# Kernel tuning notes

Measured on AMD Instinct MI355X. Metric: run time of the kernel, lower is better.

## Reference

```python
import jax, jax.numpy as jnp
import numpy as np

N_NODES = 50000
N_EDGES = 800000
IN_DIM = 128
OUT_DIM = 64
NEG_SLOPE = 0.2  # PyG GATConv default negative_slope


def setup_inputs() -> dict:
    key = jax.random.key(0)
    k1, k2, k3, k4, k5, k6 = jax.random.split(key, 6)
    x = jax.random.normal(k1, (N_NODES, IN_DIM), dtype=jnp.float32)
    edge_index = jax.random.randint(k2, (2, N_EDGES), 0, N_NODES, dtype=jnp.int32)
    # GATConv params (heads=1): linear weight, attention vectors, bias
    s = 1.0 / np.sqrt(IN_DIM)
    W = jax.random.uniform(k3, (IN_DIM, OUT_DIM), jnp.float32, -s, s)
    att_src = jax.random.normal(k4, (OUT_DIM,), jnp.float32) * 0.1
    att_dst = jax.random.normal(k5, (OUT_DIM,), jnp.float32) * 0.1
    bias = jnp.zeros((OUT_DIM,), jnp.float32)
    return {"x": x, "edge_index": edge_index, "W": W,
            "att_src": att_src, "att_dst": att_dst, "bias": bias}


def reference(x, edge_index, W, att_src, att_dst, bias):
    N = x.shape[0]
    h = x @ W  # [N, F_out]
    # add self loops (PyG GATConv default)
    loop = jnp.arange(N, dtype=edge_index.dtype)
    src = jnp.concatenate([edge_index[0], loop])  # message sources j
    dst = jnp.concatenate([edge_index[1], loop])  # aggregation targets i
    # per-node attention logits, gathered per edge
    a_src = h @ att_src  # [N]
    a_dst = h @ att_dst  # [N]
    e = jax.nn.leaky_relu(a_src[src] + a_dst[dst], NEG_SLOPE)  # [E+N]
    # scatter-softmax over incoming edges of each dst node
    m = jax.ops.segment_max(e, dst, num_segments=N)  # [N]
    ex = jnp.exp(e - m[dst])
    denom = jax.ops.segment_sum(ex, dst, num_segments=N)  # [N], >0 due to self loops
    alpha = ex / denom[dst]  # [E+N]
    # gather-weight-scatter aggregate
    out = jax.ops.segment_sum(h[src] * alpha[:, None], dst, num_segments=N)
    return out + bias
```

## Files before the change

### kernel.cpp

```cpp
#include <hip/hip_runtime.h>
#include <hip/hip_fp16.h>

#define NN 50000
#define NE 800000
#define IN_DIM 128
#define OUT_DIM 64
#define NEG 0.2f

#define BSHIFT 7
#define BNODES 128
#define NBUCK 391
#define HALFCAP 2560
#define CHUNK 4096
#define BIN_BLOCKS 196
#define GEMM_BLOCKS 391

#define XS_STRIDE 136

typedef short short8 __attribute__((ext_vector_type(8)));
typedef float f32x4 __attribute__((ext_vector_type(4)));

__device__ __forceinline__ unsigned short f2bf(float f) {
    unsigned u = __float_as_uint(f);
    u += 0x7FFFu + ((u >> 16) & 1u);
    return (unsigned short)(u >> 16);
}

__global__ __launch_bounds__(512) void gat_zero(int* __restrict__ bucket_cur) {
    if (threadIdx.x < NBUCK) bucket_cur[threadIdx.x] = 0;
}

__global__ __launch_bounds__(512) void gat_gemm_bin(
    const float* __restrict__ x, const float* __restrict__ W,
    const float* __restrict__ att_src, const float* __restrict__ att_dst,
    const int* __restrict__ src, const int* __restrict__ dst,
    unsigned short* __restrict__ h2, float* __restrict__ a_src,
    float* __restrict__ a_dst,
    int* __restrict__ gbucket, int* __restrict__ bucket_cur)
{
    __shared__ __align__(16) unsigned short xs[128 * XS_STRIDE];
    __shared__ __align__(16) unsigned short wt[64 * XS_STRIDE];
    const int tid = threadIdx.x;
    const int lane = tid & 63, wid = tid >> 6;

    if (blockIdx.x < BIN_BLOCKS) {
        int* recs_in  = (int*)xs;
        int* bcnt     = recs_in + CHUNK;
        int* cur      = bcnt + 512;
        int* lbase    = cur + 512;
        int* comb     = lbase + 512;
        int* wsum     = comb + 512;
        int* recs_out = (int*)wt;
        const int e0 = blockIdx.x * CHUNK;
        const int total = (e0 + CHUNK < NE ? CHUNK : NE - e0);

        bcnt[tid] = 0;
        __syncthreads();
#pragma unroll
        for (int k = 0; k < CHUNK / 512; ++k) {
            const int e = e0 + k * 512 + tid;
            if (e < NE) {
                const int d = dst[e];
                const int bkt = d >> BSHIFT;
                recs_in[k * 512 + tid] =
                    (bkt << 23) | (src[e] << BSHIFT) | (d & (BNODES - 1));
                atomicAdd(&bcnt[bkt], 1);
            }
        }
        __syncthreads();
        const int v = bcnt[tid];
        int incl = v;
#pragma unroll
        for (int off = 1; off < 64; off <<= 1) {
            const int n = __shfl_up(incl, off, 64);
            if (lane >= off) incl += n;
        }
        if (lane == 63) wsum[wid] = incl;
        __syncthreads();
        int wpre = 0;
#pragma unroll
        for (int w = 0; w < 8; ++w)
            if (w < wid) wpre += wsum[w];
        const int excl = wpre + incl - v;
        lbase[tid] = excl; cur[tid] = excl;
        int gb = 0;
        if (tid < NBUCK && v) gb = atomicAdd(&bucket_cur[tid], v);
        comb[tid] = gb - excl;
        __syncthreads();
#pragma unroll
        for (int k = 0; k < CHUNK / 512; ++k) {
            const int idx = k * 512 + tid;
            if (idx < total) {
                const int r = recs_in[idx];
                const unsigned bkt = (unsigned)r >> 23;
                const int pos = atomicAdd(&cur[bkt], 1);
                recs_out[pos] = r;
            }
        }
        __syncthreads();
        for (int j = tid; j < total; j += 512) {
            const int r = recs_out[j];
            const unsigned bkt = (unsigned)r >> 23;
            const int rel = comb[bkt] + j;
            if (rel < HALFCAP)
                gbucket[bkt * HALFCAP + rel] = r & 0x7FFFFF;
        }
        return;
    }

    const int block_row = (blockIdx.x - BIN_BLOCKS) * 128;

    for (int t = tid; t < 128 * 32; t += 512) {
        const int r = t >> 5, k = (t & 31) << 2;
        const int row = block_row + r;
        float4 v = make_float4(0.f, 0.f, 0.f, 0.f);
        if (row < NN) v = *(const float4*)(x + (size_t)row * IN_DIM + k);
        ushort4 p;
        p.x = f2bf(v.x); p.y = f2bf(v.y); p.z = f2bf(v.z); p.w = f2bf(v.w);
        *(ushort4*)&xs[r * XS_STRIDE + k] = p;
    }
    for (int t = tid; t < 128 * 16; t += 512) {
        const int k = t >> 4, n4 = (t & 15) << 2;
        const float4 v = *(const float4*)(W + k * 64 + n4);
        wt[(n4 + 0) * XS_STRIDE + k] = f2bf(v.x);
        wt[(n4 + 1) * XS_STRIDE + k] = f2bf(v.y);
        wt[(n4 + 2) * XS_STRIDE + k] = f2bf(v.z);
        wt[(n4 + 3) * XS_STRIDE + k] = f2bf(v.w);
    }
    __syncthreads();

    const int m = lane & 15, quad = lane >> 4;

    f32x4 acc[4];
#pragma unroll
    for (int ct = 0; ct < 4; ++ct) acc[ct] = (f32x4){0.f, 0.f, 0.f, 0.f};

    const unsigned short* xrow = &xs[(wid * 16 + m) * XS_STRIDE + quad * 8];
#pragma unroll
    for (int kt = 0; kt < 4; ++kt) {
        short8 af = *(const short8*)(xrow + kt * 32);
#pragma unroll
        for (int ct = 0; ct < 4; ++ct) {
            short8 bf = *(const short8*)(&wt[(ct * 16 + m) * XS_STRIDE + kt * 32 + quad * 8]);
            acc[ct] = __builtin_amdgcn_mfma_f32_16x16x32_bf16(af, bf, acc[ct], 0, 0, 0);
        }
    }

    float as_c[4], ad_c[4];
#pragma unroll
    for (int ct = 0; ct < 4; ++ct) {
        as_c[ct] = att_src[ct * 16 + m];
        ad_c[ct] = att_dst[ct * 16 + m];
    }
    float ps[4], pd[4];
#pragma unroll
    for (int reg = 0; reg < 4; ++reg) {
        float s = 0.f, d = 0.f;
#pragma unroll
        for (int ct = 0; ct < 4; ++ct) {
            s += acc[ct][reg] * as_c[ct];
            d += acc[ct][reg] * ad_c[ct];
        }
        ps[reg] = s; pd[reg] = d;
    }
#pragma unroll
    for (int off = 1; off < 16; off <<= 1) {
#pragma unroll
        for (int reg = 0; reg < 4; ++reg) {
            ps[reg] += __shfl_xor(ps[reg], off, 64);
            pd[reg] += __shfl_xor(pd[reg], off, 64);
        }
    }
    if (m == 0) {
#pragma unroll
        for (int reg = 0; reg < 4; ++reg) {
            const int row = block_row + wid * 16 + quad * 4 + reg;
            if (row < NN) { a_src[row] = ps[reg]; a_dst[row] = pd[reg]; }
        }
    }

    __syncthreads();
    unsigned short* hs = xs;
#pragma unroll
    for (int ct = 0; ct < 4; ++ct)
#pragma unroll
        for (int reg = 0; reg < 4; ++reg)
            hs[(wid * 16 + quad * 4 + reg) * 72 + ct * 16 + m] =
                __half_as_ushort(__float2half(acc[ct][reg]));
    __syncthreads();
    {
        const int r = tid >> 2, c = (tid & 3) * 16;
        const int row = block_row + r;
        if (row < NN) {
            uint4 v0 = *(const uint4*)&hs[r * 72 + c];
            uint4 v1 = *(const uint4*)&hs[r * 72 + c + 8];
            *(uint4*)(h2 + (size_t)row * 64 + c) = v0;
            *(uint4*)(h2 + (size_t)row * 64 + c + 8) = v1;
        }
    }
}

__global__ __launch_bounds__(1024) void gat_sortagg(
    const int* __restrict__ gbucket, const int* __restrict__ bucket_cur,
    const __half* __restrict__ h2, const float* __restrict__ a_src,
    const float* __restrict__ a_dst, const float* __restrict__ bias,
    float* __restrict__ out)
{
    __shared__ int raw[HALFCAP];
    __shared__ unsigned srtex[HALFCAP];
    __shared__ int hist[BNODES];
    __shared__ int scanb[BNODES];
    __shared__ int cur[BNODES];
    __shared__ float ads[BNODES];
    __shared__ float ass[BNODES];
    __shared__ int wsum[2];
    const int b = blockIdx.x;
    const int tid = threadIdx.x;
    const int node0 = b << BSHIFT;

    int cnt_b = bucket_cur[b];
    if (cnt_b > HALFCAP) cnt_b = HALFCAP;
    const int* win = gbucket + (size_t)b * HALFCAP;

    if (tid < BNODES) {
        hist[tid] = 0;
        const int n = node0 + tid;
        ads[tid] = (n < NN) ? a_dst[n] : 0.f;
        ass[tid] = (n < NN) ? a_src[n] : 0.f;
    }
    __syncthreads();
    for (int i = tid; i < cnt_b; i += 1024) {
        const int r = win[i];
        raw[i] = r;
        atomicAdd(&hist[r & (BNODES - 1)], 1);
    }
    __syncthreads();
    const int lane = tid & 63;
    int v = 0, incl = 0;
    if (tid < BNODES) {
        v = hist[tid];
        incl = v;
#pragma unroll
        for (int off = 1; off < 64; off <<= 1) {
            const int n = __shfl_up(incl, off, 64);
            if (lane >= off) incl += n;
        }
        if (lane == 63) wsum[tid >> 6] = incl;
    }
    __syncthreads();
    if (tid < BNODES) {
        const int inclT = incl + ((tid >= 64) ? wsum[0] : 0);
        scanb[tid] = inclT;
        cur[tid] = inclT - v;
    }
    __syncthreads();
    for (int i = tid; i < cnt_b; i += 1024) {
        const int r = raw[i];
        const int dl = r & (BNODES - 1);
        const int s = (r >> BSHIFT) & 0xFFFF;
        float ev = a_src[s] + ads[dl];
        ev = ev > 0.f ? ev : NEG * ev;
        const float ex = __expf(ev);
        const int pos = atomicAdd(&cur[dl], 1);
        srtex[pos] = (unsigned)s |
                     ((unsigned)__half_as_ushort(__float2half(ex)) << 16);
    }
    __syncthreads();

    const int wid = tid >> 6;
    const int grp = lane >> 3;
    const int cq = lane & 7;

    for (int k = 0; k < 8; ++k) {
        const int ln = k * 16 + wid;
        const int node = node0 + ln;
        if (node >= NN) break;
        const int deg = hist[ln];
        const int rbase = scanb[ln] - deg;

        float v2 = ass[ln] + ads[ln];
        v2 = v2 > 0.f ? v2 : NEG * v2;
        const float exs = __expf(v2);
        const float w0 = (grp == 0) ? exs : 0.f;

        uint4 hp = *(const uint4*)(h2 + ((size_t)node << 6) + (cq << 3));

        int   sA = -1; float eA = 0.f; uint4 gA = make_uint4(0, 0, 0, 0);
        int   sB = -1; float eB = 0.f; uint4 gB = make_uint4(0, 0, 0, 0);
        if (grp < deg) {
            const unsigned p = srtex[rbase + grp];
            sA = (int)(p & 0xffffu);
            eA = __half2float(__ushort_as_half((unsigned short)(p >> 16)));
            gA = *(const uint4*)(h2 + ((size_t)sA << 6) + (cq << 3));
        }
        if (8 + grp < deg) {
            const unsigned p = srtex[rbase + 8 + grp];
            sB = (int)(p & 0xffffu);
            eB = __half2float(__ushort_as_half((unsigned short)(p >> 16)));
            gB = *(const uint4*)(h2 + ((size_t)sB << 6) + (cq << 3));
        }

        float acc[8];
        {
            const __half2* hh = (const __half2*)&hp;
#pragma unroll
            for (int j = 0; j < 4; ++j) {
                float2 f = __half22float2(hh[j]);
                acc[2 * j] = w0 * f.x;
                acc[2 * j + 1] = w0 * f.y;
            }
        }
        float den = w0;

        for (int base = 0; base < deg; base += 8) {
            int sC = -1; float eC = 0.f; uint4 gC = make_uint4(0, 0, 0, 0);
            const int en = base + 16 + grp;
            if (en < deg) {
                const unsigned p = srtex[rbase + en];
                sC = (int)(p & 0xffffu);
                eC = __half2float(__ushort_as_half((unsigned short)(p >> 16)));
                gC = *(const uint4*)(h2 + ((size_t)sC << 6) + (cq << 3));
            }
            if (sA >= 0) {
                const __half2* gh = (const __half2*)&gA;
#pragma unroll
                for (int j = 0; j < 4; ++j) {
                    float2 f = __half22float2(gh[j]);
                    acc[2 * j] += eA * f.x;
                    acc[2 * j + 1] += eA * f.y;
                }
                den += eA;
            }
            sA = sB; eA = eB; gA = gB;
            sB = sC; eB = eC; gB = gC;
        }

#pragma unroll
        for (int off = 8; off < 64; off <<= 1) {
#pragma unroll
            for (int j = 0; j < 8; ++j) acc[j] += __shfl_xor(acc[j], off, 64);
            den += __shfl_xor(den, off, 64);
        }

        if (grp == 0) {
            const float inv = 1.f / den;
            const float4 b0 = *(const float4*)(bias + (cq << 3));
            const float4 b1 = *(const float4*)(bias + (cq << 3) + 4);
            float4 o0, o1;
            o0.x = acc[0] * inv + b0.x; o0.y = acc[1] * inv + b0.y;
            o0.z = acc[2] * inv + b0.z; o0.w = acc[3] * inv + b0.w;
            o1.x = acc[4] * inv + b1.x; o1.y = acc[5] * inv + b1.y;
            o1.z = acc[6] * inv + b1.z; o1.w = acc[7] * inv + b1.w;
            float* op = out + ((size_t)node << 6) + (cq << 3);
            *(float4*)op = o0;
            *(float4*)(op + 4) = o1;
        }
    }
}

extern "C" void kernel_launch(void* const* d_in, const int* in_sizes, int n_in,
                              void* d_out, int out_size, void* d_ws, size_t ws_size,
                              hipStream_t stream) {
    const float* x       = (const float*)d_in[0];
    const int*   eidx    = (const int*)d_in[1];
    const float* W       = (const float*)d_in[2];
    const float* att_src = (const float*)d_in[3];
    const float* att_dst = (const float*)d_in[4];
    const float* bias    = (const float*)d_in[5];
    float* out = (float*)d_out;

    unsigned short* h2 = (unsigned short*)d_ws;
    int*   gbucket = (int*)((char*)d_ws + (size_t)NN * OUT_DIM * 2);
    float* a_src   = (float*)(gbucket + (size_t)NBUCK * HALFCAP);
    float* a_dst   = a_src + NN;
    int*   bucket_cur = (int*)(a_dst + NN);

    const int* src = eidx;
    const int* dst = eidx + NE;

    gat_zero<<<1, 512, 0, stream>>>(bucket_cur);
    gat_gemm_bin<<<GEMM_BLOCKS + BIN_BLOCKS, 512, 0, stream>>>(
        x, W, att_src, att_dst, src, dst, h2, a_src, a_dst, gbucket, bucket_cur);
    gat_sortagg<<<NBUCK, 1024, 0, stream>>>(
        gbucket, bucket_cur, (const __half*)h2, a_src, a_dst, bias, out);
}
```

Measured before the change: 125.7 us.

## Assign one 8-lane group per node instead of one wave per node in aggregation

The aggregation phase previously used one 64-lane wave per destination node, with eight 8-lane groups splitting the node's edges and a cross-group shuffle reduction at the end. Now each 8-lane group owns one node (128 nodes across the 1024-thread block) and walks all of that node's edges serially, prefetching two edges ahead. This removes the shuffle reduction and the idle lanes on low-degree nodes (average degree is about 16). In exchange, each lane runs a longer serial loop, and work becomes imbalanced across lanes within a wave when node degrees differ.

Measured after the change: 113.1 us. -10.0%, faster.

```diff
diff --git a/kernel.cpp b/kernel.cpp
--- a/kernel.cpp
+++ b/kernel.cpp
@@ -267,82 +267,69 @@
     }
     __syncthreads();
 
-    const int wid = tid >> 6;
-    const int grp = lane >> 3;
-    const int cq = lane & 7;
-
-    for (int k = 0; k < 8; ++k) {
-        const int ln = k * 16 + wid;
-        const int node = node0 + ln;
-        if (node >= NN) break;
-        const int deg = hist[ln];
-        const int rbase = scanb[ln] - deg;
-
-        float v2 = ass[ln] + ads[ln];
-        v2 = v2 > 0.f ? v2 : NEG * v2;
-        const float exs = __expf(v2);
-        const float w0 = (grp == 0) ? exs : 0.f;
-
-        uint4 hp = *(const uint4*)(h2 + ((size_t)node << 6) + (cq << 3));
-
-        int   sA = -1; float eA = 0.f; uint4 gA = make_uint4(0, 0, 0, 0);
-        int   sB = -1; float eB = 0.f; uint4 gB = make_uint4(0, 0, 0, 0);
-        if (grp < deg) {
-            const unsigned p = srtex[rbase + grp];
-            sA = (int)(p & 0xffffu);
-            eA = __half2float(__ushort_as_half((unsigned short)(p >> 16)));
-            gA = *(const uint4*)(h2 + ((size_t)sA << 6) + (cq << 3));
-        }
-        if (8 + grp < deg) {
-            const unsigned p = srtex[rbase + 8 + grp];
-            sB = (int)(p & 0xffffu);
-            eB = __half2float(__ushort_as_half((unsigned short)(p >> 16)));
-            gB = *(const uint4*)(h2 + ((size_t)sB << 6) + (cq << 3));
-        }
-
-        float acc[8];
-        {
-            const __half2* hh = (const __half2*)&hp;
-#pragma unroll
-            for (int j = 0; j < 4; ++j) {
-                float2 f = __half22float2(hh[j]);
-                acc[2 * j] = w0 * f.x;
-                acc[2 * j + 1] = w0 * f.y;
-            }
-        }
-        float den = w0;
-
-        for (int base = 0; base < deg; base += 8) {
-            int sC = -1; float eC = 0.f; uint4 gC = make_uint4(0, 0, 0, 0);
-            const int en = base + 16 + grp;
-            if (en < deg) {
-                const unsigned p = srtex[rbase + en];
-                sC = (int)(p & 0xffffu);
-                eC = __half2float(__ushort_as_half((unsigned short)(p >> 16)));
-                gC = *(const uint4*)(h2 + ((size_t)sC << 6) + (cq << 3));
-            }
-            if (sA >= 0) {
-                const __half2* gh = (const __half2*)&gA;
+    {
+        const int g  = tid >> 3;
+        const int cq = tid & 7;
+        const int node = node0 + g;
+        if (node < NN) {
+            const int deg = hist[g];
+            const int rbase = scanb[g] - deg;
+
+            float v2 = ass[g] + ads[g];
+            v2 = v2 > 0.f ? v2 : NEG * v2;
+            const float exs = __expf(v2);
+
+            uint4 hp = *(const uint4*)(h2 + ((size_t)node << 6) + (cq << 3));
+
+            float eA = 0.f, eB = 0.f;
+            uint4 gA = make_uint4(0, 0, 0, 0), gB = make_uint4(0, 0, 0, 0);
+            if (0 < deg) {
+                const unsigned p = srtex[rbase];
+                const int s = (int)(p & 0xffffu);
+                eA = __half2float(__ushort_as_half((unsigned short)(p >> 16)));
+                gA = *(const uint4*)(h2 + ((size_t)s << 6) + (cq << 3));
+            }
+            if (1 < deg) {
+                const unsigned p = srtex[rbase + 1];
+                const int s = (int)(p & 0xffffu);
+                eB = __half2float(__ushort_as_half((unsigned short)(p >> 16)));
+                gB = *(const uint4*)(h2 + ((size_t)s << 6) + (cq << 3));
+            }
+
+            float acc[8];
+            {
+                const __half2* hh = (const __half2*)&hp;
 #pragma unroll
                 for (int j = 0; j < 4; ++j) {
-                    float2 f = __half22float2(gh[j]);
-                    acc[2 * j] += eA * f.x;
-                    acc[2 * j + 1] += eA * f.y;
+                    float2 f = __half22float2(hh[j]);
+                    acc[2 * j]     = exs * f.x;
+                    acc[2 * j + 1] = exs * f.y;
                 }
-                den += eA;
-            }
-            sA = sB; eA = eB; gA = gB;
-            sB = sC; eB = eC; gB = gC;
-        }
-
-#pragma unroll
-        for (int off = 8; off < 64; off <<= 1) {
-#pragma unroll
-            for (int j = 0; j < 8; ++j) acc[j] += __shfl_xor(acc[j], off, 64);
-            den += __shfl_xor(den, off, 64);
-        }
-
-        if (grp == 0) {
+            }
+            float den = exs;
+
+            for (int i = 0; i < deg; ++i) {
+                float eC = 0.f; uint4 gC = make_uint4(0, 0, 0, 0);
+                if (i + 2 < deg) {
+                    const unsigned p = srtex[rbase + i + 2];
+                    const int s = (int)(p & 0xffffu);
+                    eC = __half2float(__ushort_as_half((unsigned short)(p >> 16)));
+                    gC = *(const uint4*)(h2 + ((size_t)s << 6) + (cq << 3));
+                }
+                {
+                    const __half2* gh = (const __half2*)&gA;
+#pragma unroll
+                    for (int j = 0; j < 4; ++j) {
+                        float2 f = __half22float2(gh[j]);
+                        acc[2 * j]     += eA * f.x;
+                        acc[2 * j + 1] += eA * f.y;
+                    }
+                    den += eA;
+                }
+                eA = eB; gA = gB;
+                eB = eC; gB = gC;
+            }
+
             const float inv = 1.f / den;
             const float4 b0 = *(const float4*)(bias + (cq << 3));
             const float4 b1 = *(const float4*)(bias + (cq << 3) + 4);
```
